# Kernel optimization log

Hardware: AMD Instinct MI355X
Metric: run time of the kernel (lower is better)

Reference implementation:

```python
import jax, jax.numpy as jnp
import numpy as np

N = 100000   # num nodes
E = 1600000  # num edges
D = 64       # feature / hidden dim (irreps_in == hidden_dim)
SCALE = D ** -0.5


def setup_inputs() -> dict:
    key = jax.random.key(0)
    ks = jax.random.split(key, 6)
    x = jax.random.normal(ks[0], (N, D), dtype=jnp.float32)
    edge_index = jax.random.randint(ks[1], (2, E), 0, N, dtype=jnp.int32)
    std = D ** -0.5
    Wq = jax.random.normal(ks[2], (D, D), dtype=jnp.float32) * std
    Wk = jax.random.normal(ks[3], (D, D), dtype=jnp.float32) * std
    Wv = jax.random.normal(ks[4], (D, D), dtype=jnp.float32) * std
    Wo = jax.random.normal(ks[5], (D, D), dtype=jnp.float32) * std
    return {"x": x, "edge_index": edge_index, "Wq": Wq, "Wk": Wk, "Wv": Wv, "Wo": Wo}


def reference(x, edge_index, Wq, Wk, Wv, Wo):
    # Per-receiver variable-length attention over incoming neighbors.
    # Mathematically identical to the torch module's degree-bucketed SDPA
    # (softmax over each node's neighbor set), without padding buffers.
    sender, receiver = edge_index[0], edge_index[1]
    Q = x @ Wq  # [N, D]
    K = x @ Wk
    V = x @ Wv
    # per-edge logits: <Q[receiver], K[sender]> * scale
    s = jnp.einsum('ed,ed->e', Q[receiver], K[sender]) * SCALE  # [E]
    # numerically stable segment softmax over receiver groups
    m = jax.ops.segment_max(s, receiver, num_segments=N)  # -inf for empty segments
    m_safe = jnp.where(jnp.isfinite(m), m, 0.0)
    p = jnp.exp(s - m_safe[receiver])  # [E]
    denom = jax.ops.segment_sum(p, receiver, num_segments=N)  # [N]
    num = jax.ops.segment_sum(p[:, None] * V[sender], receiver, num_segments=N)  # [N, D]
    # zero-degree nodes get out = 0 (matches torch: skipped buckets + nan_to_num)
    out = jnp.where(denom[:, None] > 0,
                    num / jnp.maximum(denom, 1e-30)[:, None],
                    0.0)
    return x + out @ Wo
```

## Files before the change

kernel.cpp:

```cpp
#include <hip/hip_runtime.h>
#include <hip/hip_bf16.h>

#define DIM 64
#define SCALE 0.125f
#define BINSH 5
#define NPB 32
#define BCAP 768
#define DBSH 8
#define NDB 256
#define CBCAP 4864
#define CHUNKA 8192
#define MAXCB 512

static __device__ __forceinline__ unsigned int pack2bf(float a, float b) {
    unsigned int ua = __float_as_uint(a), ub = __float_as_uint(b);
    ua += 0x7fffu + ((ua >> 16) & 1u);
    ub += 0x7fffu + ((ub >> 16) & 1u);
    return (ua >> 16) | (ub & 0xffff0000u);
}
static __device__ __forceinline__ float2 unpack2bf(unsigned int u) {
    return make_float2(__uint_as_float(u << 16), __uint_as_float(u & 0xffff0000u));
}

__global__ __launch_bounds__(1024) void k_prepA(const int* __restrict__ send,
                                                const int* __restrict__ recv,
                                                const float* __restrict__ Wv,
                                                const float* __restrict__ Wo,
                                                float* __restrict__ Wvo,
                                                int* __restrict__ bucketCur,
                                                unsigned int* __restrict__ cbuf,
                                                int E, int NCB) {
    __shared__ __align__(16) unsigned int elist[CHUNKA];
    __shared__ int hist[MAXCB];
    __shared__ int lofs[MAXCB + 1];
    __shared__ int gbase[MAXCB];
    __shared__ int lcur[MAXCB];
    __shared__ int wsum[8];
    int tid = threadIdx.x;
    int lane = tid & 63;

    if (blockIdx.x == 0) {
        float* av = (float*)elist;
        float* bo = (float*)elist + 4096;
        ((float4*)av)[tid] = ((const float4*)Wv)[tid];
        ((float4*)bo)[tid] = ((const float4*)Wo)[tid];
        __syncthreads();
        int r = tid >> 4, c0 = (tid & 15) * 4;
        float acc[4] = {0.f, 0.f, 0.f, 0.f};
        for (int k = 0; k < 64; k++) {
            float a = av[r * 64 + k];
#pragma unroll
            for (int j = 0; j < 4; j++) acc[j] = fmaf(a, bo[k * 64 + c0 + j], acc[j]);
        }
#pragma unroll
        for (int j = 0; j < 4; j++) Wvo[r * 64 + c0 + j] = acc[j];
        __syncthreads();
    }

    int base = blockIdx.x * CHUNKA;
    int lim = min(base + CHUNKA, E);
    int cnt = lim - base;

    for (int i = tid; i < NCB; i += 1024) hist[i] = 0;
    __syncthreads();
    for (int i = base + tid; i < lim; i += 1024)
        atomicAdd(&hist[recv[i] >> DBSH], 1);
    __syncthreads();

    {
        int d = (tid < NCB) ? hist[tid] : 0;
        int incl = d;
        for (int o = 1; o < 64; o <<= 1) {
            int t2 = __shfl_up(incl, o, 64);
            if (lane >= o) incl += t2;
        }
        if (tid < 512 && lane == 63) wsum[tid >> 6] = incl;
        __syncthreads();
        if (tid == 0) {
            int a = 0;
#pragma unroll
            for (int i2 = 0; i2 < 8; i2++) { int v = wsum[i2]; wsum[i2] = a; a += v; }
        }
        __syncthreads();
        if (tid < NCB) {
            int excl = incl - d + wsum[tid >> 6];
            lofs[tid] = excl;
            lcur[tid] = excl;
            gbase[tid] = d ? atomicAdd(&bucketCur[tid], d) : 0;
        }
        if (tid == 0) lofs[NCB] = cnt;
    }
    __syncthreads();

    for (int i = base + tid; i < lim; i += 1024) {
        int r = recv[i];
        int b = r >> DBSH;
        int p = atomicAdd(&lcur[b], 1);
        elist[p] = (unsigned)send[i] | ((unsigned)(r & (NDB - 1)) << 17);
    }
    __syncthreads();

    for (int i = tid; i < cnt; i += 1024) {
        int lo = 0, hi = NCB;
        while (hi - lo > 1) {
            int mid = (lo + hi) >> 1;
            if (lofs[mid] <= i) lo = mid; else hi = mid;
        }
        int pos = gbase[lo] + (i - lofs[lo]);
        if (pos < CBCAP)
            cbuf[(size_t)lo * CBCAP + pos] = elist[i];
    }
}

__global__ __launch_bounds__(256) void k_fused(const float* __restrict__ x,
                                               const float* __restrict__ Wq,
                                               const float* __restrict__ Wk,
                                               const float* __restrict__ Wvo,
                                               const int* __restrict__ bucketCur,
                                               unsigned int* __restrict__ cbuf,
                                               int* __restrict__ nstart,
                                               int* __restrict__ ncount,
                                               float* __restrict__ Q,
                                               unsigned int* __restrict__ KVb,
                                               int N, int NCB, int nchunk) {
    __shared__ __align__(16) float smem[8192];
    int tid = threadIdx.x;
    int wv = tid >> 6;
    int lane = tid & 63;

    if ((int)blockIdx.x < NCB) {
        int b = blockIdx.x;
        int bbase = b * CBCAP;
        int cnt = min(bucketCur[b], CBCAP);
        unsigned int* elist = (unsigned int*)smem;
        int* ldeg = (int*)smem + CBCAP;
        int* lcur = ldeg + NDB;
        int* wsum = lcur + NDB;

        for (int i = tid; i < cnt; i += 256) elist[i] = cbuf[bbase + i];
        ldeg[tid] = 0;
        __syncthreads();
        for (int i = tid; i < cnt; i += 256)
            atomicAdd(&ldeg[(elist[i] >> 17) & (NDB - 1)], 1);
        __syncthreads();

        int d = ldeg[tid];
        int incl = d;
        for (int o = 1; o < 64; o <<= 1) {
            int t = __shfl_up(incl, o, 64);
            if (lane >= o) incl += t;
        }
        if (lane == 63) wsum[wv] = incl;
        __syncthreads();
        int woff = 0;
        for (int w2 = 0; w2 < wv; w2++) woff += wsum[w2];
        int start = woff + incl - d;
        lcur[tid] = start;
        int r = (b << DBSH) + tid;
        if (r < N) {
            nstart[r] = bbase + start;
            ncount[r] = d;
        }
        __syncthreads();

        for (int i = tid; i < cnt; i += 256) {
            unsigned u = elist[i];
            int n = (u >> 17) & (NDB - 1);
            int p = atomicAdd(&lcur[n], 1);
            cbuf[bbase + p] = u & 0x1FFFFu;
        }
        return;
    }

    int qb = blockIdx.x - NCB;
    int m = qb / nchunk;
    int cb = qb % nchunk;
    const float* W = (m == 0) ? Wq : ((m == 1) ? Wk : Wvo);

    int base = cb * 256 + wv * 64;
    if (base < N) {
        float* xw = smem + wv * 2048;
        int lr = lane >> 3;
        int lc = lane & 7;
        const float* xp = xw + lr * 8;

        float acc[8][8];
#pragma unroll
        for (int i = 0; i < 8; i++)
#pragma unroll
            for (int j = 0; j < 8; j++) acc[i][j] = 0.f;

#pragma unroll
        for (int h = 0; h < 2; h++) {
#pragma unroll
            for (int c4 = 0; c4 < 8; c4++) {
                float4 v = make_float4(0.f, 0.f, 0.f, 0.f);
                if (base + lane < N)
                    v = ((const float4*)x)[(size_t)(base + lane) * 16 + h * 8 + c4];
                xw[(c4 * 4 + 0) * 64 + lane] = v.x;
                xw[(c4 * 4 + 1) * 64 + lane] = v.y;
                xw[(c4 * 4 + 2) * 64 + lane] = v.z;
                xw[(c4 * 4 + 3) * 64 + lane] = v.w;
            }
            asm volatile("s_waitcnt lgkmcnt(0)" ::: "memory");

            const float* wp = W + h * 2048 + lc * 8;

            float4 xa = *(const float4*)(xp);
            float4 xb = *(const float4*)(xp + 4);
            float4 wa0 = *(const float4*)(wp);
            float4 wb0 = *(const float4*)(wp + 4);
            float4 wa1 = *(const float4*)(wp + 64);
            float4 wb1 = *(const float4*)(wp + 68);
#pragma unroll 4
            for (int kk = 0; kk < 32; kk++) {
                float4 xan, xbn, wan, wbn;
                if (kk < 31) {
                    xan = *(const float4*)(xp + (kk + 1) * 64);
                    xbn = *(const float4*)(xp + (kk + 1) * 64 + 4);
                }
                if (kk < 30) {
                    wan = *(const float4*)(wp + (kk + 2) * 64);
                    wbn = *(const float4*)(wp + (kk + 2) * 64 + 4);
                }
                float xv[8] = {xa.x, xa.y, xa.z, xa.w, xb.x, xb.y, xb.z, xb.w};
                float wc[8] = {wa0.x, wa0.y, wa0.z, wa0.w, wb0.x, wb0.y, wb0.z, wb0.w};
#pragma unroll
                for (int i = 0; i < 8; i++)
#pragma unroll
                    for (int j = 0; j < 8; j++)
                        acc[i][j] = fmaf(xv[i], wc[j], acc[i][j]);
                xa = xan; xb = xbn;
                wa0 = wa1; wb0 = wb1;
                wa1 = wan; wb1 = wbn;
            }
        }

#pragma unroll
        for (int i = 0; i < 8; i++) {
            int row = base + lr * 8 + i;
            if (row < N) {
                if (m == 0) {
                    float* dst = &Q[(size_t)row * 64 + lc * 8];
                    ((float4*)dst)[0] = make_float4(acc[i][0], acc[i][1], acc[i][2], acc[i][3]);
                    ((float4*)dst)[1] = make_float4(acc[i][4], acc[i][5], acc[i][6], acc[i][7]);
                } else {
                    unsigned int* dst = &KVb[(size_t)row * 64 + (m - 1) * 32 + lc * 4];
                    uint4 pk;
                    pk.x = pack2bf(acc[i][0], acc[i][1]);
                    pk.y = pack2bf(acc[i][2], acc[i][3]);
                    pk.z = pack2bf(acc[i][4], acc[i][5]);
                    pk.w = pack2bf(acc[i][6], acc[i][7]);
                    *((uint4*)dst) = pk;
                }
            }
        }
    }
}

__global__ __launch_bounds__(256) void k_attn(const float* __restrict__ Q,
                                              const unsigned int* __restrict__ KVb,
                                              const float* __restrict__ x,
                                              const int* __restrict__ nstart,
                                              const int* __restrict__ ncount,
                                              const unsigned int* __restrict__ nlist,
                                              float* __restrict__ out, int N) {
    __shared__ unsigned int llist[BCAP];
    __shared__ int lofs[NPB + 1];
    __shared__ int sbs;
    int tid = threadIdx.x;
    int wv = tid >> 6;
    int lane = tid & 63;
    int g = lane >> 3;
    int sub = lane & 7;

    int j = blockIdx.x;
    int r0 = j << BINSH;

    if (tid == 0) sbs = nstart[r0];
    __syncthreads();
    int sbase = sbs;
    if (tid < NPB) {
        int r = r0 + tid;
        lofs[tid] = min(nstart[r] - sbase, BCAP);
        if (tid == NPB - 1)
            lofs[NPB] = min(nstart[r] + ncount[r] - sbase, BCAP);
    }
    __syncthreads();
    int cnt = lofs[NPB];
    for (int i = tid; i < cnt; i += 256) llist[i] = nlist[sbase + i];
    __syncthreads();

    for (int n = wv; n < NPB; n += 4) {
        int r = r0 + n;
        if (r >= N) break;
        int start = lofs[n];
        int end = lofs[n + 1];
        float4 qa = *((const float4*)&Q[(size_t)r * 64 + sub * 8]);
        float4 qb = *((const float4*)&Q[(size_t)r * 64 + sub * 8 + 4]);
        float q[8] = {qa.x, qa.y, qa.z, qa.w, qb.x, qb.y, qb.z, qb.w};
        float acc[8] = {0.f, 0.f, 0.f, 0.f, 0.f, 0.f, 0.f, 0.f};
        float dpart = 0.f;

        int eA = start + g;
        bool vA = eA < end;
        unsigned int sA = vA ? llist[eA] : 0u;
        uint4 kA = *((const uint4*)&KVb[(size_t)sA * 64 + sub * 4]);
        uint4 uA = *((const uint4*)&KVb[(size_t)sA * 64 + 32 + sub * 4]);
        int eB = start + 8 + g;
        bool vB = eB < end;
        unsigned int sB = vB ? llist[eB] : 0u;
        uint4 kB = *((const uint4*)&KVb[(size_t)sB * 64 + sub * 4]);
        uint4 uB = *((const uint4*)&KVb[(size_t)sB * 64 + 32 + sub * 4]);

        for (int bb = start; bb < end; bb += 8) {
            int eC = bb + 16 + g;
            bool vC = eC < end;
            unsigned int sC = vC ? llist[eC] : 0u;
            uint4 kC = *((const uint4*)&KVb[(size_t)sC * 64 + sub * 4]);
            uint4 uC = *((const uint4*)&KVb[(size_t)sC * 64 + 32 + sub * 4]);

            float2 k01 = unpack2bf(kA.x), k23 = unpack2bf(kA.y);
            float2 k45 = unpack2bf(kA.z), k67 = unpack2bf(kA.w);
            float dot = q[0] * k01.x + q[1] * k01.y + q[2] * k23.x + q[3] * k23.y
                      + q[4] * k45.x + q[5] * k45.y + q[6] * k67.x + q[7] * k67.y;
            dot += __shfl_xor(dot, 1);
            dot += __shfl_xor(dot, 2);
            dot += __shfl_xor(dot, 4);
            float w = vA ? __expf(dot * SCALE) : 0.f;

            float2 v01 = unpack2bf(uA.x), v23 = unpack2bf(uA.y);
            float2 v45 = unpack2bf(uA.z), v67 = unpack2bf(uA.w);
            acc[0] = fmaf(w, v01.x, acc[0]);
            acc[1] = fmaf(w, v01.y, acc[1]);
            acc[2] = fmaf(w, v23.x, acc[2]);
            acc[3] = fmaf(w, v23.y, acc[3]);
            acc[4] = fmaf(w, v45.x, acc[4]);
            acc[5] = fmaf(w, v45.y, acc[5]);
            acc[6] = fmaf(w, v67.x, acc[6]);
            acc[7] = fmaf(w, v67.y, acc[7]);
            dpart += w;

            kA = kB; uA = uB; vA = vB;
            kB = kC; uB = uC; vB = vC;
        }

        dpart += __shfl_xor(dpart, 8); dpart += __shfl_xor(dpart, 16); dpart += __shfl_xor(dpart, 32);
#pragma unroll
        for (int jj = 0; jj < 8; jj++) {
            acc[jj] += __shfl_xor(acc[jj], 8);
            acc[jj] += __shfl_xor(acc[jj], 16);
            acc[jj] += __shfl_xor(acc[jj], 32);
        }

        float inv = (dpart > 0.f) ? (1.0f / dpart) : 0.f;

        if (g == 0) {
            float4 xa = *((const float4*)&x[(size_t)r * 64 + sub * 8]);
            float4 xb = *((const float4*)&x[(size_t)r * 64 + sub * 8 + 4]);
            float4 oa = make_float4(fmaf(acc[0], inv, xa.x), fmaf(acc[1], inv, xa.y),
                                    fmaf(acc[2], inv, xa.z), fmaf(acc[3], inv, xa.w));
            float4 ob = make_float4(fmaf(acc[4], inv, xb.x), fmaf(acc[5], inv, xb.y),
                                    fmaf(acc[6], inv, xb.z), fmaf(acc[7], inv, xb.w));
            *((float4*)&out[(size_t)r * 64 + sub * 8]) = oa;
            *((float4*)&out[(size_t)r * 64 + sub * 8 + 4]) = ob;
        }
    }
}


extern "C" void kernel_launch(void* const* d_in, const int* in_sizes, int n_in,
                              void* d_out, int out_size, void* d_ws, size_t ws_size,
                              hipStream_t stream) {
    const float* x  = (const float*)d_in[0];
    const int* edge = (const int*)d_in[1];
    const float* Wq = (const float*)d_in[2];
    const float* Wk = (const float*)d_in[3];
    const float* Wv = (const float*)d_in[4];
    const float* Wo = (const float*)d_in[5];
    float* out = (float*)d_out;

    int N = in_sizes[0] / DIM;
    int E = in_sizes[1] / 2;
    int NBK = (N + NPB - 1) >> BINSH;
    int NCB = (N + NDB - 1) >> DBSH;

    char* p = (char*)d_ws;
    auto cv = [&](size_t bytes) {
        char* r = p;
        p += ((bytes + 255) / 256) * 256;
        return r;
    };
    float*        Q         = (float*)cv((size_t)N * 64 * 4);
    unsigned int* KVb       = (unsigned int*)cv((size_t)N * 64 * 4);
    float*        Wvo       = (float*)cv(64 * 64 * 4);
    int*          bucketCur = (int*)cv((size_t)NCB * 4);
    unsigned int* cbuf      = (unsigned int*)cv((size_t)NCB * CBCAP * 4);
    int*          nstart    = (int*)cv((size_t)N * 4);
    int*          ncount    = (int*)cv((size_t)N * 4);
    (void)ws_size; (void)n_in; (void)out_size;

    const int* send = edge;
    const int* recv = edge + E;

    int NBA = (E + CHUNKA - 1) / CHUNKA;
    int nchunk = (N + 255) / 256;

    hipMemsetAsync(bucketCur, 0, (size_t)NCB * 4, stream);
    k_prepA<<<NBA, 1024, 0, stream>>>(send, recv, Wv, Wo, Wvo, bucketCur, cbuf, E, NCB);
    k_fused<<<NCB + 3 * nchunk, 256, 0, stream>>>(x, Wq, Wk, Wvo, bucketCur, cbuf,
                                                  nstart, ncount, Q, KVb,
                                                  N, NCB, nchunk);
    k_attn<<<NBK, 256, 0, stream>>>(Q, KVb, x, nstart, ncount, cbuf, out, N);
}
```

Baseline: 230.8 us.

## Merge edge bucketing with projections and sort nodes inside attention kernel

Folds the coarse edge bucketing into the same launch as the Q/K/V GEMM blocks, so the two stages run concurrently in one kernel. Each V-projection block now recomputes Wv·Wo in shared memory instead of relying on a separate prep step. The per-node fine sort moves into the attention kernel: each attention block rescans its coarse bucket and builds its local neighbour list in shared memory, which removes the nstart/ncount arrays and one kernel launch. The cost is that each coarse bucket is scanned eight times in attention, the Wvo product is recomputed per block, and the prep blocks shrink from 1024 to 256 threads.

Result: slower. 246.1 us (+6.6%).

```diff
diff --git a/kernel.cpp b/kernel.cpp
--- a/kernel.cpp
+++ b/kernel.cpp
@@ -10,7 +10,7 @@
 #define NDB 256
 #define CBCAP 4864
 #define CHUNKA 8192
-#define MAXCB 512
+#define MAXCB 400
 
 static __device__ __forceinline__ unsigned int pack2bf(float a, float b) {
     unsigned int ua = __float_as_uint(a), ub = __float_as_uint(b);
@@ -22,174 +22,165 @@
     return make_float2(__uint_as_float(u << 16), __uint_as_float(u & 0xffff0000u));
 }
 
-__global__ __launch_bounds__(1024) void k_prepA(const int* __restrict__ send,
-                                                const int* __restrict__ recv,
-                                                const float* __restrict__ Wv,
-                                                const float* __restrict__ Wo,
-                                                float* __restrict__ Wvo,
-                                                int* __restrict__ bucketCur,
-                                                unsigned int* __restrict__ cbuf,
-                                                int E, int NCB) {
-    __shared__ __align__(16) unsigned int elist[CHUNKA];
-    __shared__ int hist[MAXCB];
-    __shared__ int lofs[MAXCB + 1];
-    __shared__ int gbase[MAXCB];
-    __shared__ int lcur[MAXCB];
-    __shared__ int wsum[8];
+__global__ __launch_bounds__(256) void k_pg(const int* __restrict__ send,
+                                            const int* __restrict__ recv,
+                                            const float* __restrict__ x,
+                                            const float* __restrict__ Wq,
+                                            const float* __restrict__ Wk,
+                                            const float* __restrict__ Wv,
+                                            const float* __restrict__ Wo,
+                                            int* __restrict__ bucketCur,
+                                            unsigned int* __restrict__ cbuf,
+                                            float* __restrict__ Q,
+                                            unsigned int* __restrict__ KVb,
+                                            int E, int N, int NCB,
+                                            int NBA, int nchunk) {
+    __shared__ __align__(16) float smem[10240];
     int tid = threadIdx.x;
+    int wvv = tid >> 6;
     int lane = tid & 63;
 
-    if (blockIdx.x == 0) {
-        float* av = (float*)elist;
-        float* bo = (float*)elist + 4096;
-        ((float4*)av)[tid] = ((const float4*)Wv)[tid];
-        ((float4*)bo)[tid] = ((const float4*)Wo)[tid];
-        __syncthreads();
-        int r = tid >> 4, c0 = (tid & 15) * 4;
-        float acc[4] = {0.f, 0.f, 0.f, 0.f};
-        for (int k = 0; k < 64; k++) {
-            float a = av[r * 64 + k];
-#pragma unroll
-            for (int j = 0; j < 4; j++) acc[j] = fmaf(a, bo[k * 64 + c0 + j], acc[j]);
-        }
-#pragma unroll
-        for (int j = 0; j < 4; j++) Wvo[r * 64 + c0 + j] = acc[j];
-        __syncthreads();
-    }
-
-    int base = blockIdx.x * CHUNKA;
-    int lim = min(base + CHUNKA, E);
-    int cnt = lim - base;
-
-    for (int i = tid; i < NCB; i += 1024) hist[i] = 0;
-    __syncthreads();
-    for (int i = base + tid; i < lim; i += 1024)
-        atomicAdd(&hist[recv[i] >> DBSH], 1);
-    __syncthreads();
-
-    {
-        int d = (tid < NCB) ? hist[tid] : 0;
-        int incl = d;
+    if ((int)blockIdx.x < NBA) {
+        unsigned int* elist = (unsigned int*)smem;
+        int* hist  = (int*)(elist + CHUNKA);
+        int* lofs  = hist + MAXCB;
+        int* gbase = lofs + MAXCB + 1;
+        int* lcur  = gbase + MAXCB;
+        int* wsum  = lcur + MAXCB;
+
+        int base = blockIdx.x * CHUNKA;
+        int lim = min(base + CHUNKA, E);
+        int cnt = lim - base;
+
+        for (int i = tid; i < NCB; i += 256) hist[i] = 0;
+        __syncthreads();
+        for (int i = base + tid; i < lim; i += 256)
+            atomicAdd(&hist[recv[i] >> DBSH], 1);
+        __syncthreads();
+
+        int i0 = 2 * tid, i1 = 2 * tid + 1;
+        int h0 = (i0 < NCB) ? hist[i0] : 0;
+        int h1 = (i1 < NCB) ? hist[i1] : 0;
+        int ps = h0 + h1;
+        int incl = ps;
         for (int o = 1; o < 64; o <<= 1) {
             int t2 = __shfl_up(incl, o, 64);
             if (lane >= o) incl += t2;
         }
-        if (tid < 512 && lane == 63) wsum[tid >> 6] = incl;
+        if (lane == 63) wsum[wvv] = incl;
         __syncthreads();
         if (tid == 0) {
             int a = 0;
 #pragma unroll
-            for (int i2 = 0; i2 < 8; i2++) { int v = wsum[i2]; wsum[i2] = a; a += v; }
-        }
-        __syncthreads();
-        if (tid < NCB) {
-            int excl = incl - d + wsum[tid >> 6];
-            lofs[tid] = excl;
-            lcur[tid] = excl;
-            gbase[tid] = d ? atomicAdd(&bucketCur[tid], d) : 0;
+            for (int i2 = 0; i2 < 4; i2++) { int v = wsum[i2]; wsum[i2] = a; a += v; }
+        }
+        __syncthreads();
+        int excl = incl - ps + wsum[wvv];
+        if (i0 < NCB) {
+            lofs[i0] = excl; lcur[i0] = excl;
+            gbase[i0] = h0 ? atomicAdd(&bucketCur[i0], h0) : 0;
+        }
+        if (i1 < NCB) {
+            lofs[i1] = excl + h0; lcur[i1] = excl + h0;
+            gbase[i1] = h1 ? atomicAdd(&bucketCur[i1], h1) : 0;
         }
         if (tid == 0) lofs[NCB] = cnt;
-    }
-    __syncthreads();
-
-    for (int i = base + tid; i < lim; i += 1024) {
-        int r = recv[i];
-        int b = r >> DBSH;
-        int p = atomicAdd(&lcur[b], 1);
-        elist[p] = (unsigned)send[i] | ((unsigned)(r & (NDB - 1)) << 17);
-    }
-    __syncthreads();
-
-    for (int i = tid; i < cnt; i += 1024) {
-        int lo = 0, hi = NCB;
-        while (hi - lo > 1) {
-            int mid = (lo + hi) >> 1;
-            if (lofs[mid] <= i) lo = mid; else hi = mid;
-        }
-        int pos = gbase[lo] + (i - lofs[lo]);
-        if (pos < CBCAP)
-            cbuf[(size_t)lo * CBCAP + pos] = elist[i];
-    }
-}
-
-__global__ __launch_bounds__(256) void k_fused(const float* __restrict__ x,
-                                               const float* __restrict__ Wq,
-                                               const float* __restrict__ Wk,
-                                               const float* __restrict__ Wvo,
-                                               const int* __restrict__ bucketCur,
-                                               unsigned int* __restrict__ cbuf,
-                                               int* __restrict__ nstart,
-                                               int* __restrict__ ncount,
-                                               float* __restrict__ Q,
-                                               unsigned int* __restrict__ KVb,
-                                               int N, int NCB, int nchunk) {
-    __shared__ __align__(16) float smem[8192];
-    int tid = threadIdx.x;
-    int wv = tid >> 6;
-    int lane = tid & 63;
-
-    if ((int)blockIdx.x < NCB) {
-        int b = blockIdx.x;
-        int bbase = b * CBCAP;
-        int cnt = min(bucketCur[b], CBCAP);
-        unsigned int* elist = (unsigned int*)smem;
-        int* ldeg = (int*)smem + CBCAP;
-        int* lcur = ldeg + NDB;
-        int* wsum = lcur + NDB;
-
-        for (int i = tid; i < cnt; i += 256) elist[i] = cbuf[bbase + i];
-        ldeg[tid] = 0;
-        __syncthreads();
-        for (int i = tid; i < cnt; i += 256)
-            atomicAdd(&ldeg[(elist[i] >> 17) & (NDB - 1)], 1);
-        __syncthreads();
-
-        int d = ldeg[tid];
-        int incl = d;
-        for (int o = 1; o < 64; o <<= 1) {
-            int t = __shfl_up(incl, o, 64);
-            if (lane >= o) incl += t;
-        }
-        if (lane == 63) wsum[wv] = incl;
-        __syncthreads();
-        int woff = 0;
-        for (int w2 = 0; w2 < wv; w2++) woff += wsum[w2];
-        int start = woff + incl - d;
-        lcur[tid] = start;
-        int r = (b << DBSH) + tid;
-        if (r < N) {
-            nstart[r] = bbase + start;
-            ncount[r] = d;
+        __syncthreads();
+
+        for (int i = base + tid; i < lim; i += 256) {
+            int r = recv[i];
+            int b = r >> DBSH;
+            int p = atomicAdd(&lcur[b], 1);
+            elist[p] = (unsigned)send[i] | ((unsigned)(r & (NDB - 1)) << 17);
         }
         __syncthreads();
 
         for (int i = tid; i < cnt; i += 256) {
-            unsigned u = elist[i];
-            int n = (u >> 17) & (NDB - 1);
-            int p = atomicAdd(&lcur[n], 1);
-            cbuf[bbase + p] = u & 0x1FFFFu;
+            int lo = 0, hi = NCB;
+            while (hi - lo > 1) {
+                int mid = (lo + hi) >> 1;
+                if (lofs[mid] <= i) lo = mid; else hi = mid;
+            }
+            int pos = gbase[lo] + (i - lofs[lo]);
+            if (pos < CBCAP)
+                cbuf[(size_t)lo * CBCAP + pos] = elist[i];
         }
         return;
     }
 
-    int qb = blockIdx.x - NCB;
+    int qb = blockIdx.x - NBA;
     int m = qb / nchunk;
     int cb = qb % nchunk;
-    const float* W = (m == 0) ? Wq : ((m == 1) ? Wk : Wvo);
-
-    int base = cb * 256 + wv * 64;
-    if (base < N) {
-        float* xw = smem + wv * 2048;
-        int lr = lane >> 3;
-        int lc = lane & 7;
+    int base = cb * 256 + wvv * 64;
+    int lr = lane >> 3;
+    int lc = lane & 7;
+
+    float acc[8][8];
+#pragma unroll
+    for (int i = 0; i < 8; i++)
+#pragma unroll
+        for (int j = 0; j < 8; j++) acc[i][j] = 0.f;
+
+    if (m == 2) {
+        float* av = smem;
+        float* bo = smem + 4096;
+        for (int i = tid; i < 1024; i += 256) {
+            ((float4*)av)[i] = ((const float4*)Wv)[i];
+            ((float4*)bo)[i] = ((const float4*)Wo)[i];
+        }
+        __syncthreads();
+        int rr = tid >> 2, c0 = (tid & 3) * 16;
+        float wvo[16];
+#pragma unroll
+        for (int j = 0; j < 16; j++) wvo[j] = 0.f;
+        for (int k = 0; k < 64; k++) {
+            float a = av[rr * 64 + k];
+#pragma unroll
+            for (int j = 0; j < 16; j++)
+                wvo[j] = fmaf(a, bo[k * 64 + c0 + j], wvo[j]);
+        }
+        __syncthreads();
+#pragma unroll
+        for (int j = 0; j < 16; j++) smem[rr * 64 + c0 + j] = wvo[j];
+        __syncthreads();
+
+        if (base < N) {
+            float* xw = smem + 4096 + wvv * 1024;
+            const float* xp = xw + lr * 8;
+#pragma unroll
+            for (int h = 0; h < 4; h++) {
+#pragma unroll
+                for (int c4 = 0; c4 < 4; c4++) {
+                    float4 v = make_float4(0.f, 0.f, 0.f, 0.f);
+                    if (base + lane < N)
+                        v = ((const float4*)x)[(size_t)(base + lane) * 16 + h * 4 + c4];
+                    xw[(c4 * 4 + 0) * 64 + lane] = v.x;
+                    xw[(c4 * 4 + 1) * 64 + lane] = v.y;
+                    xw[(c4 * 4 + 2) * 64 + lane] = v.z;
+                    xw[(c4 * 4 + 3) * 64 + lane] = v.w;
+                }
+                asm volatile("s_waitcnt lgkmcnt(0)" ::: "memory");
+                const float* wp = smem + (h * 16) * 64 + lc * 8;
+#pragma unroll 4
+                for (int kk = 0; kk < 16; kk++) {
+                    float4 xa = *(const float4*)(xp + kk * 64);
+                    float4 xb = *(const float4*)(xp + kk * 64 + 4);
+                    float4 wa = *(const float4*)(wp + kk * 64);
+                    float4 wb = *(const float4*)(wp + kk * 64 + 4);
+                    float xv[8] = {xa.x, xa.y, xa.z, xa.w, xb.x, xb.y, xb.z, xb.w};
+                    float wc[8] = {wa.x, wa.y, wa.z, wa.w, wb.x, wb.y, wb.z, wb.w};
+#pragma unroll
+                    for (int i = 0; i < 8; i++)
+#pragma unroll
+                        for (int j = 0; j < 8; j++)
+                            acc[i][j] = fmaf(xv[i], wc[j], acc[i][j]);
+                }
+            }
+        }
+    } else if (base < N) {
+        const float* W = (m == 0) ? Wq : Wk;
+        float* xw = smem + wvv * 2048;
         const float* xp = xw + lr * 8;
-
-        float acc[8][8];
-#pragma unroll
-        for (int i = 0; i < 8; i++)
-#pragma unroll
-            for (int j = 0; j < 8; j++) acc[i][j] = 0.f;
-
 #pragma unroll
         for (int h = 0; h < 2; h++) {
 #pragma unroll
@@ -205,7 +196,6 @@
             asm volatile("s_waitcnt lgkmcnt(0)" ::: "memory");
 
             const float* wp = W + h * 2048 + lc * 8;
-
             float4 xa = *(const float4*)(xp);
             float4 xb = *(const float4*)(xp + 4);
             float4 wa0 = *(const float4*)(wp);
@@ -235,7 +225,9 @@
                 wa1 = wan; wb1 = wbn;
             }
         }
-
+    }
+
+    if (base < N) {
 #pragma unroll
         for (int i = 0; i < 8; i++) {
             int row = base + lr * 8 + i;
@@ -261,38 +253,58 @@
 __global__ __launch_bounds__(256) void k_attn(const float* __restrict__ Q,
                                               const unsigned int* __restrict__ KVb,
                                               const float* __restrict__ x,
-                                              const int* __restrict__ nstart,
-                                              const int* __restrict__ ncount,
-                                              const unsigned int* __restrict__ nlist,
+                                              const int* __restrict__ bucketCur,
+                                              const unsigned int* __restrict__ cbuf,
                                               float* __restrict__ out, int N) {
     __shared__ unsigned int llist[BCAP];
-    __shared__ int lofs[NPB + 1];
-    __shared__ int sbs;
+    __shared__ int ldeg[NPB], lofs[NPB + 1], lcur[NPB];
     int tid = threadIdx.x;
-    int wv = tid >> 6;
+    int wvv = tid >> 6;
     int lane = tid & 63;
     int g = lane >> 3;
     int sub = lane & 7;
 
     int j = blockIdx.x;
-    int r0 = j << BINSH;
-
-    if (tid == 0) sbs = nstart[r0];
+    int b = j >> 3;
+    int s = j & 7;
+    size_t bbase = (size_t)b * CBCAP;
+    int cnt = min(bucketCur[b], CBCAP);
+
+    if (tid < NPB) ldeg[tid] = 0;
     __syncthreads();
-    int sbase = sbs;
-    if (tid < NPB) {
-        int r = r0 + tid;
-        lofs[tid] = min(nstart[r] - sbase, BCAP);
-        if (tid == NPB - 1)
-            lofs[NPB] = min(nstart[r] + ncount[r] - sbase, BCAP);
+
+    for (int i = tid; i < cnt; i += 256) {
+        unsigned u = cbuf[bbase + i];
+        int n = (u >> 17) & (NDB - 1);
+        if ((n >> 5) == s) atomicAdd(&ldeg[n & (NPB - 1)], 1);
     }
     __syncthreads();
-    int cnt = lofs[NPB];
-    for (int i = tid; i < cnt; i += 256) llist[i] = nlist[sbase + i];
+
+    if (wvv == 0 && lane < NPB) {
+        int d = ldeg[lane];
+        int sc = d;
+        for (int o = 1; o < NPB; o <<= 1) {
+            int t = __shfl_up(sc, o, NPB);
+            if (lane >= o) sc += t;
+        }
+        lofs[lane + 1] = min(sc, BCAP);
+        lcur[lane] = min(sc - d, BCAP);
+        if (lane == 0) lofs[0] = 0;
+    }
     __syncthreads();
 
-    for (int n = wv; n < NPB; n += 4) {
-        int r = r0 + n;
+    for (int i = tid; i < cnt; i += 256) {
+        unsigned u = cbuf[bbase + i];
+        int n = (u >> 17) & (NDB - 1);
+        if ((n >> 5) == s) {
+            int p = atomicAdd(&lcur[n & (NPB - 1)], 1);
+            if (p < BCAP) llist[p] = u & 0x1FFFFu;
+        }
+    }
+    __syncthreads();
+
+    for (int n = wvv; n < NPB; n += 4) {
+        int r = (j << BINSH) + n;
         if (r >= N) break;
         int start = lofs[n];
         int end = lofs[n + 1];
@@ -393,11 +405,8 @@
     };
     float*        Q         = (float*)cv((size_t)N * 64 * 4);
     unsigned int* KVb       = (unsigned int*)cv((size_t)N * 64 * 4);
-    float*        Wvo       = (float*)cv(64 * 64 * 4);
     int*          bucketCur = (int*)cv((size_t)NCB * 4);
     unsigned int* cbuf      = (unsigned int*)cv((size_t)NCB * CBCAP * 4);
-    int*          nstart    = (int*)cv((size_t)N * 4);
-    int*          ncount    = (int*)cv((size_t)N * 4);
     (void)ws_size; (void)n_in; (void)out_size;
 
     const int* send = edge;
@@ -407,9 +416,8 @@
     int nchunk = (N + 255) / 256;
 
     hipMemsetAsync(bucketCur, 0, (size_t)NCB * 4, stream);
-    k_prepA<<<NBA, 1024, 0, stream>>>(send, recv, Wv, Wo, Wvo, bucketCur, cbuf, E, NCB);
-    k_fused<<<NCB + 3 * nchunk, 256, 0, stream>>>(x, Wq, Wk, Wvo, bucketCur, cbuf,
-                                                  nstart, ncount, Q, KVb,
-                                                  N, NCB, nchunk);
-    k_attn<<<NBK, 256, 0, stream>>>(Q, KVb, x, nstart, ncount, cbuf, out, N);
+    k_pg<<<NBA + 3 * nchunk, 256, 0, stream>>>(send, recv, x, Wq, Wk, Wv, Wo,
+                                               bucketCur, cbuf, Q, KVb,
+                                               E, N, NCB, NBA, nchunk);
+    k_attn<<<NBK, 256, 0, stream>>>(Q, KVb, x, bucketCur, cbuf, out, N);
 }
```

## Double-buffer x tile in LDS with register prefetch in projection GEMM

Applied to the files above, without the earlier changes.

The projection part of the fused kernel now stages x in eight-column slices through a two-slot LDS ring per wave, instead of transposing half the row block (32 columns) at a time. The global loads for the next slice are issued into registers before the current slice's FMAs run, so load latency can overlap compute. LDS per block drops from 32 KB to 22 KB, which may allow more resident blocks. In exchange there are more LDS write phases and waitcnt points, and x is now read from LDS per k-step rather than through a register prefetch.

Result: slower. 248.3 us (+7.6%).

```diff
diff --git a/kernel.cpp b/kernel.cpp
--- a/kernel.cpp
+++ b/kernel.cpp
@@ -123,9 +123,9 @@
                                                float* __restrict__ Q,
                                                unsigned int* __restrict__ KVb,
                                                int N, int NCB, int nchunk) {
-    __shared__ __align__(16) float smem[8192];
+    __shared__ __align__(16) float smem[5632];
     int tid = threadIdx.x;
-    int wv = tid >> 6;
+    int wvv = tid >> 6;
     int lane = tid & 63;
 
     if ((int)blockIdx.x < NCB) {
@@ -150,10 +150,10 @@
             int t = __shfl_up(incl, o, 64);
             if (lane >= o) incl += t;
         }
-        if (lane == 63) wsum[wv] = incl;
+        if (lane == 63) wsum[wvv] = incl;
         __syncthreads();
         int woff = 0;
-        for (int w2 = 0; w2 < wv; w2++) woff += wsum[w2];
+        for (int w2 = 0; w2 < wvv; w2++) woff += wsum[w2];
         int start = woff + incl - d;
         lcur[tid] = start;
         int r = (b << DBSH) + tid;
@@ -177,12 +177,15 @@
     int cb = qb % nchunk;
     const float* W = (m == 0) ? Wq : ((m == 1) ? Wk : Wvo);
 
-    int base = cb * 256 + wv * 64;
+    int base = cb * 256 + wvv * 64;
     if (base < N) {
-        float* xw = smem + wv * 2048;
+        float* xw = smem + wvv * 1024;
         int lr = lane >> 3;
         int lc = lane & 7;
-        const float* xp = xw + lr * 8;
+        const float* wp = W + lc * 8;
+        bool rowok = (base + lane) < N;
+        const float4* xrow = (const float4*)x + (size_t)(base + lane) * 16;
+        const float4 z4 = make_float4(0.f, 0.f, 0.f, 0.f);
 
         float acc[8][8];
 #pragma unroll
@@ -190,39 +193,37 @@
 #pragma unroll
             for (int j = 0; j < 8; j++) acc[i][j] = 0.f;
 
-#pragma unroll
-        for (int h = 0; h < 2; h++) {
-#pragma unroll
-            for (int c4 = 0; c4 < 8; c4++) {
-                float4 v = make_float4(0.f, 0.f, 0.f, 0.f);
-                if (base + lane < N)
-                    v = ((const float4*)x)[(size_t)(base + lane) * 16 + h * 8 + c4];
-                xw[(c4 * 4 + 0) * 64 + lane] = v.x;
-                xw[(c4 * 4 + 1) * 64 + lane] = v.y;
-                xw[(c4 * 4 + 2) * 64 + lane] = v.z;
-                xw[(c4 * 4 + 3) * 64 + lane] = v.w;
-            }
-            asm volatile("s_waitcnt lgkmcnt(0)" ::: "memory");
-
-            const float* wp = W + h * 2048 + lc * 8;
-
-            float4 xa = *(const float4*)(xp);
-            float4 xb = *(const float4*)(xp + 4);
-            float4 wa0 = *(const float4*)(wp);
-            float4 wb0 = *(const float4*)(wp + 4);
-            float4 wa1 = *(const float4*)(wp + 64);
-            float4 wb1 = *(const float4*)(wp + 68);
-#pragma unroll 4
-            for (int kk = 0; kk < 32; kk++) {
-                float4 xan, xbn, wan, wbn;
-                if (kk < 31) {
-                    xan = *(const float4*)(xp + (kk + 1) * 64);
-                    xbn = *(const float4*)(xp + (kk + 1) * 64 + 4);
+        {
+            float4 c0 = rowok ? xrow[0] : z4;
+            float4 c1 = rowok ? xrow[1] : z4;
+            float* b0 = xw;
+            b0[0 * 64 + lane] = c0.x; b0[1 * 64 + lane] = c0.y;
+            b0[2 * 64 + lane] = c0.z; b0[3 * 64 + lane] = c0.w;
+            b0[4 * 64 + lane] = c1.x; b0[5 * 64 + lane] = c1.y;
+            b0[6 * 64 + lane] = c1.z; b0[7 * 64 + lane] = c1.w;
+        }
+        float4 n0 = rowok ? xrow[2] : z4;
+        float4 n1 = rowok ? xrow[3] : z4;
+
+        float4 wa0 = *(const float4*)(wp);
+        float4 wb0 = *(const float4*)(wp + 4);
+        float4 wa1 = *(const float4*)(wp + 64);
+        float4 wb1 = *(const float4*)(wp + 68);
+
+        asm volatile("s_waitcnt lgkmcnt(0)" ::: "memory");
+
+        for (int h = 0; h < 8; h++) {
+            const float* xp = xw + (h & 1) * 512 + lr * 8;
+#pragma unroll
+            for (int kk = 0; kk < 8; kk++) {
+                int k = h * 8 + kk;
+                float4 wan, wbn;
+                if (k < 62) {
+                    wan = *(const float4*)(wp + (k + 2) * 64);
+                    wbn = *(const float4*)(wp + (k + 2) * 64 + 4);
                 }
-                if (kk < 30) {
-                    wan = *(const float4*)(wp + (kk + 2) * 64);
-                    wbn = *(const float4*)(wp + (kk + 2) * 64 + 4);
-                }
+                float4 xa = *(const float4*)(xp + kk * 64);
+                float4 xb = *(const float4*)(xp + kk * 64 + 4);
                 float xv[8] = {xa.x, xa.y, xa.z, xa.w, xb.x, xb.y, xb.z, xb.w};
                 float wc[8] = {wa0.x, wa0.y, wa0.z, wa0.w, wb0.x, wb0.y, wb0.z, wb0.w};
 #pragma unroll
@@ -230,9 +231,20 @@
 #pragma unroll
                     for (int j = 0; j < 8; j++)
                         acc[i][j] = fmaf(xv[i], wc[j], acc[i][j]);
-                xa = xan; xb = xbn;
                 wa0 = wa1; wb0 = wb1;
                 wa1 = wan; wb1 = wbn;
+            }
+            if (h < 7) {
+                float* nb = xw + ((h + 1) & 1) * 512;
+                nb[0 * 64 + lane] = n0.x; nb[1 * 64 + lane] = n0.y;
+                nb[2 * 64 + lane] = n0.z; nb[3 * 64 + lane] = n0.w;
+                nb[4 * 64 + lane] = n1.x; nb[5 * 64 + lane] = n1.y;
+                nb[6 * 64 + lane] = n1.z; nb[7 * 64 + lane] = n1.w;
+                if (h < 6) {
+                    n0 = rowok ? xrow[(h + 2) * 2] : z4;
+                    n1 = rowok ? xrow[(h + 2) * 2 + 1] : z4;
+                }
+                asm volatile("s_waitcnt lgkmcnt(0)" ::: "memory");
             }
         }
 
```
